# Optimization experiments

Hardware: AMD Instinct MI355X
Metric: run time of the kernel (lower is better)

Reference implementation:

```python
import jax, jax.numpy as jnp
import numpy as np
import math

VOCAB, D, H, L = 32000, 1024, 16, 4
HD = D // H
DFF = 4 * D
EPS = 1e-5


def setup_inputs() -> dict:
    key = jax.random.key(0)
    ks = jax.random.split(key, 20)
    B, T = 4, 1024
    s = 0.02
    inp = {
        'inputs': jax.random.randint(ks[0], (B, T), 0, VOCAB),
        'emb_table': jax.random.normal(ks[1], (VOCAB, D), jnp.float32) * s,
        'Wq': jax.random.normal(ks[2], (L, D, D), jnp.float32) * s,
        'bq': jnp.zeros((L, D), jnp.float32),
        'Wk': jax.random.normal(ks[3], (L, D, D), jnp.float32) * s,
        'bk': jnp.zeros((L, D), jnp.float32),
        'Wv': jax.random.normal(ks[4], (L, D, D), jnp.float32) * s,
        'bv': jnp.zeros((L, D), jnp.float32),
        'Wo': jax.random.normal(ks[5], (L, D, D), jnp.float32) * s,
        'bo': jnp.zeros((L, D), jnp.float32),
        'ln1_g': jnp.ones((L, D), jnp.float32),
        'ln1_b': jnp.zeros((L, D), jnp.float32),
        'W1': jax.random.normal(ks[6], (L, D, DFF), jnp.float32) * s,
        'b1': jnp.zeros((L, DFF), jnp.float32),
        'W2': jax.random.normal(ks[7], (L, DFF, D), jnp.float32) * s,
        'b2': jnp.zeros((L, D), jnp.float32),
        'ln2_g': jnp.ones((L, D), jnp.float32),
        'ln2_b': jnp.zeros((L, D), jnp.float32),
    }
    return inp


def _layernorm(x, g, b):
    mu = jnp.mean(x, axis=-1, keepdims=True)
    var = jnp.mean(jnp.square(x - mu), axis=-1, keepdims=True)
    return (x - mu) * jax.lax.rsqrt(var + EPS) * g + b


def _pos_emb(T):
    pos = jnp.arange(T, dtype=jnp.float32)[:, None]          # [T,1]
    div = jnp.exp(jnp.arange(0, D, 2, dtype=jnp.float32) * (-math.log(10000.0) / D))
    pe = jnp.zeros((T, D), jnp.float32)
    pe = pe.at[:, 0::2].set(jnp.sin(pos * div))
    pe = pe.at[:, 1::2].set(jnp.cos(pos * div))
    return pe


def reference(inputs, emb_table, Wq, bq, Wk, bk, Wv, bv, Wo, bo,
              ln1_g, ln1_b, W1, b1, W2, b2, ln2_g, ln2_b):
    B, T = inputs.shape
    x = emb_table[inputs] + _pos_emb(T)[None, :, :]          # [B,T,D]
    causal = jnp.tril(jnp.ones((T, T), bool))                # [T,T]
    scale = 1.0 / math.sqrt(HD)
    for l in range(L):
        q = (x @ Wq[l] + bq[l]).reshape(B, T, H, HD)
        k = (x @ Wk[l] + bk[l]).reshape(B, T, H, HD)
        v = (x @ Wv[l] + bv[l]).reshape(B, T, H, HD)
        scores = jnp.einsum('bqhd,bkhd->bhqk', q, k) * scale
        scores = jnp.where(causal, scores, -jnp.inf)
        w = jax.nn.softmax(scores, axis=-1)
        attn = jnp.einsum('bhqk,bkhd->bqhd', w, v).reshape(B, T, D)
        attn = attn @ Wo[l] + bo[l]
        x = _layernorm(x + attn, ln1_g[l], ln1_b[l])
        ff = jax.nn.relu(x @ W1[l] + b1[l]) @ W2[l] + b2[l]
        x = _layernorm(x + ff, ln2_g[l], ln2_b[l])
    return x
```

## Files before the change

kernel.cpp:

```cpp
#include <hip/hip_runtime.h>

typedef __attribute__((ext_vector_type(8))) __bf16 bf16x8;
typedef __attribute__((ext_vector_type(4))) float f32x4;
typedef __attribute__((ext_vector_type(8))) unsigned short ushort8;

#define DMODEL 1024
#define SEQ 1024
#define NLAYER 4

__device__ __forceinline__ unsigned short f2bf(float f) {
  unsigned u = __float_as_uint(f);
  u += 0x7fffu + ((u >> 16) & 1u);
  return (unsigned short)(u >> 16);
}

__device__ __forceinline__ void async_copy16(const void* gsrc, const void* lds_dst) {
  __builtin_amdgcn_global_load_lds(
      (__attribute__((address_space(1))) void*)(unsigned long long)(gsrc),
      (__attribute__((address_space(3))) void*)(unsigned int)(unsigned long long)(lds_dst),
      16, 0, 0);
}

__device__ __forceinline__ f32x4 mfma16(bf16x8 a, bf16x8 b, f32x4 c) {
  return __builtin_amdgcn_mfma_f32_16x16x32_bf16(a, b, c, 0, 0, 0);
}

__global__ __launch_bounds__(256) void preproc_kernel(
    const int* __restrict__ tok, const float* __restrict__ emb,
    const float* __restrict__ Wq, const float* __restrict__ Wk,
    const float* __restrict__ Wv, const float* __restrict__ Wo,
    const float* __restrict__ W1, const float* __restrict__ W2,
    const float* __restrict__ bq, const float* __restrict__ bk,
    const float* __restrict__ bv,
    unsigned short* __restrict__ wqkv_t, unsigned short* __restrict__ wo_t,
    unsigned short* __restrict__ w1_t, unsigned short* __restrict__ w2_t,
    float* __restrict__ qkvb, float* __restrict__ xf,
    unsigned short* __restrict__ xb) {
  __shared__ unsigned short tileT[64 * 136];
  const int bid = blockIdx.x;
  const int tid = threadIdx.x;
  if (bid < 6144) {
    const float* src; unsigned short* dst; size_t R, C; int tx, ty;
    if (bid < 2048) {
      int w = bid >> 9, z = (bid >> 7) & 3, tl = bid & 127;
      tx = tl & 15; ty = tl >> 4; R = 1024; C = 1024;
      if (w == 0)      { src = Wq + (size_t)z * 1048576; dst = wqkv_t + (size_t)z * 3145728; }
      else if (w == 1) { src = Wk + (size_t)z * 1048576; dst = wqkv_t + (size_t)z * 3145728 + 1048576; }
      else if (w == 2) { src = Wv + (size_t)z * 1048576; dst = wqkv_t + (size_t)z * 3145728 + 2097152; }
      else             { src = Wo + (size_t)z * 1048576; dst = wo_t + (size_t)z * 1048576; }
    } else if (bid < 4096) {
      int t = bid - 2048, z = t >> 9, tl = t & 511;
      tx = tl & 63; ty = tl >> 6; R = 1024; C = 4096;
      src = W1 + (size_t)z * 4194304; dst = w1_t + (size_t)z * 4194304;
    } else {
      int t = bid - 4096, z = t >> 9, tl = t & 511;
      tx = tl & 15; ty = tl >> 4; R = 4096; C = 1024;
      src = W2 + (size_t)z * 4194304; dst = w2_t + (size_t)z * 4194304;
    }
    const int c0 = tx * 64, r0 = ty * 128;
    const int s16 = tid & 15, hi = tid >> 4;
#pragma unroll
    for (int it = 0; it < 8; ++it) {
      const int r = it * 16 + hi;
      f32x4 v = __builtin_nontemporal_load(
          (const f32x4*)(src + (size_t)(r0 + r) * C + c0 + s16 * 4));
#pragma unroll
      for (int j = 0; j < 4; ++j)
        tileT[(s16 * 4 + j) * 136 + r] = f2bf(v[j]);
    }
    __syncthreads();
#pragma unroll
    for (int p = 0; p < 4; ++p) {
      const int c = p * 16 + hi;
      ushort8 o = *(const ushort8*)&tileT[c * 136 + s16 * 8];
      *(ushort8*)(dst + (size_t)(c0 + c) * R + r0 + s16 * 8) = o;
    }
  } else if (bid < 10240) {
    const int row = bid - 6144;
    const int t = row & (SEQ - 1);
    const int tk = tok[row];
    const int col = tid * 4;
    float4 e = *(const float4*)(emb + (size_t)tk * DMODEL + col);
    const float c = -9.21034037197618f / (float)DMODEL;
    float d0 = __expf((float)(col)*c);
    float d1 = __expf((float)(col + 2) * c);
    float a0 = (float)t * d0, a1 = (float)t * d1;
    e.x += sinf(a0); e.y += cosf(a0); e.z += sinf(a1); e.w += cosf(a1);
    *(float4*)(xf + (size_t)row * DMODEL + col) = e;
    ushort4 ub;
    ub.x = f2bf(e.x); ub.y = f2bf(e.y); ub.z = f2bf(e.z); ub.w = f2bf(e.w);
    *(ushort4*)(xb + (size_t)row * DMODEL + col) = ub;
  } else {
    int i = (bid - 10240) * 256 + tid;
    if (i < NLAYER * 3072) {
      int l = i / 3072, j = i % 3072;
      float v = (j < 1024) ? bq[l * 1024 + j]
              : (j < 2048) ? bk[l * 1024 + j - 1024]
                           : bv[l * 1024 + j - 2048];
      qkvb[i] = v;
    }
  }
}

#define G256_PHASE(BUF, MH, NH, STAGE_STMT, VM)                                   \
  {                                                                               \
    if (NH == 0) {                                                                \
      _Pragma("unroll") for (int fm = 0; fm < 4; ++fm)                            \
      _Pragma("unroll") for (int kk = 0; kk < 2; ++kk) {                          \
        int row = wr * 64 + fm * 16 + lr;                                         \
        int cb = (kk * 64 + g * 16) ^ ((row & 4) ? 32 : 0) ^ ((row & 8) ? 64 : 0);\
        af[fm][kk] = *(const bf16x8*)((const char*)&As[BUF][MH][0] + row * 128 + cb); \
      }                                                                           \
    }                                                                             \
    _Pragma("unroll") for (int fn = 0; fn < 2; ++fn)                              \
    _Pragma("unroll") for (int kk = 0; kk < 2; ++kk) {                            \
      int row = wc * 32 + fn * 16 + lr;                                           \
      int cb = (kk * 64 + g * 16) ^ ((row & 4) ? 32 : 0) ^ ((row & 8) ? 64 : 0);  \
      bfr[fn][kk] = *(const bf16x8*)((const char*)&Bs[BUF][NH][0] + row * 128 + cb); \
    }                                                                             \
    STAGE_STMT;                                                                   \
    if (VM == 1) asm volatile("s_waitcnt vmcnt(4)" ::: "memory");                 \
    if (VM == 2) asm volatile("s_waitcnt vmcnt(0)" ::: "memory");                 \
    asm volatile("s_barrier" ::: "memory");                                       \
    asm volatile("s_waitcnt lgkmcnt(0)" ::: "memory");                            \
    __builtin_amdgcn_s_setprio(1);                                                \
    _Pragma("unroll") for (int fm = 0; fm < 4; ++fm)                              \
    _Pragma("unroll") for (int fn = 0; fn < 2; ++fn)                              \
    _Pragma("unroll") for (int kk = 0; kk < 2; ++kk)                              \
      acc[MH][fm][NH][fn] = mfma16(af[fm][kk], bfr[fn][kk], acc[MH][fm][NH][fn]); \
    __builtin_amdgcn_s_setprio(0);                                                \
    asm volatile("s_barrier" ::: "memory");                                       \
  }

template <int QKV>
__global__ __launch_bounds__(512, 1) void gemm256(
    const unsigned short* __restrict__ A, const unsigned short* __restrict__ Bt,
    const float* __restrict__ bias, unsigned short* __restrict__ Cb,
    unsigned short* __restrict__ Cb2, int N) {
  __shared__ __align__(16) unsigned short As[2][2][8192];
  __shared__ __align__(16) unsigned short Bs[2][2][8192];
  constexpr int NK = 16;
  constexpr int NI = 8;

  const int tid = threadIdx.x;
  const int wid = tid >> 6, l = tid & 63;
  const int lr = l & 15, g = l >> 4;
  const int wr = wid >> 2, wc = wid & 3;

  const int gx = gridDim.x, nwg = gx * gridDim.y;
  int bid = blockIdx.y * gx + blockIdx.x;
  const int cpx = nwg >> 3;
  bid = (bid & 7) * cpx + (bid >> 3);
  const int rm = (bid / gx) * 256, rn = (bid % gx) * 256;

  const int kOff = ((l & 7) * 8) ^ ((l & 32) ? 16 : 0) ^ ((wid & 1) ? 32 : 0);
  const int rOff = wid * 8 + (l >> 3);

  auto stA = [&](int buf, int half, int t) {
#pragma unroll
    for (int r2 = 0; r2 < 2; ++r2) {
      const unsigned short* gs =
          A + (size_t)(rm + half * 128 + r2 * 64 + rOff) * 1024 + t * 64 + kOff;
      async_copy16(gs, &As[buf][half][r2 * 4096 + wid * 512]);
    }
  };
  auto stB = [&](int buf, int half, int t) {
#pragma unroll
    for (int r2 = 0; r2 < 2; ++r2) {
      const unsigned short* gs =
          Bt + (size_t)(rn + half * 128 + r2 * 64 + rOff) * 1024 + t * 64 + kOff;
      async_copy16(gs, &Bs[buf][half][r2 * 4096 + wid * 512]);
    }
  };

  f32x4 acc[2][4][2][2] = {};
  bf16x8 af[4][2], bfr[2][2];

  stA(0, 0, 0); stA(0, 1, 0); stB(0, 0, 0); stB(0, 1, 0);
  stA(1, 0, 1); stB(1, 0, 1);
  asm volatile("s_waitcnt vmcnt(4)" ::: "memory");
  asm volatile("s_barrier" ::: "memory");

  for (int i = 0; i < NI - 1; ++i) {
    const int t1 = 2 * i + 1, t2 = 2 * i + 2, t3 = 2 * i + 3;
    G256_PHASE(0, 0, 0, { stA(1, 1, t1); }, 0)
    G256_PHASE(0, 0, 1, { stB(1, 1, t1); }, 0)
    G256_PHASE(0, 1, 0, { stA(0, 0, t2); }, 0)
    G256_PHASE(0, 1, 1, { stB(0, 0, t2); }, 1)
    G256_PHASE(1, 0, 0, { stA(0, 1, t2); }, 0)
    G256_PHASE(1, 0, 1, { stB(0, 1, t2); }, 0)
    G256_PHASE(1, 1, 0, { if (t3 < NK) stA(1, 0, t3); }, 0)
    G256_PHASE(1, 1, 1, { if (t3 < NK) stB(1, 0, t3); }, 1)
  }
  {
    const int t1 = NK - 1;
    G256_PHASE(0, 0, 0, { stA(1, 1, t1); }, 0)
    G256_PHASE(0, 0, 1, { stB(1, 1, t1); }, 0)
    G256_PHASE(0, 1, 0, {}, 0)
    G256_PHASE(0, 1, 1, {}, 2)
    G256_PHASE(1, 0, 0, {}, 0)
    G256_PHASE(1, 0, 1, {}, 0)
    G256_PHASE(1, 1, 0, {}, 0)
    G256_PHASE(1, 1, 1, {}, 0)
  }

#pragma unroll
  for (int mh = 0; mh < 2; ++mh)
#pragma unroll
    for (int nh = 0; nh < 2; ++nh)
#pragma unroll
      for (int fn = 0; fn < 2; ++fn) {
        const int col = rn + nh * 128 + wc * 32 + fn * 16 + lr;
        const float bv = bias[col];
        if (QKV && col >= 2048) {
#pragma unroll
          for (int fm = 0; fm < 4; ++fm) {
            const int row0 = rm + mh * 128 + wr * 64 + fm * 16 + g * 4;
            ushort4 vv;
            vv.x = f2bf(acc[mh][fm][nh][fn][0] + bv);
            vv.y = f2bf(acc[mh][fm][nh][fn][1] + bv);
            vv.z = f2bf(acc[mh][fm][nh][fn][2] + bv);
            vv.w = f2bf(acc[mh][fm][nh][fn][3] + bv);
            *(ushort4*)(Cb2 + (size_t)(col - 2048) * 4096 + row0) = vv;
          }
        } else {
          const float sc = (QKV && col < 1024) ? 0.18033688011112042f : 1.0f;
          const int ldc = QKV ? 2048 : N;
#pragma unroll
          for (int fm = 0; fm < 4; ++fm)
#pragma unroll
            for (int r = 0; r < 4; ++r) {
              const int row = rm + mh * 128 + wr * 64 + fm * 16 + g * 4 + r;
              float v = (acc[mh][fm][nh][fn][r] + bv) * sc;
              if (!QKV) v = fmaxf(v, 0.0f);
              Cb[(size_t)row * ldc + col] = f2bf(v);
            }
        }
      }
}

__global__ __launch_bounds__(512, 4) void gemm_bf16w(
    const unsigned short* __restrict__ A, const unsigned short* __restrict__ Bt,
    const float* __restrict__ bias, float* __restrict__ Cf,
    const float* __restrict__ Xres, int N, int K) {
  __shared__ __align__(16) unsigned short As[2][8192];
  __shared__ __align__(16) unsigned short Bs[2][8192];
  const int tid = threadIdx.x;
  const int wid = tid >> 6, l = tid & 63, lr = l & 15, g = l >> 4;
  const int wr = wid >> 2, wc = wid & 3;
  const int d = blockIdx.y * 8 + blockIdx.x;
  const int xcd = d & 7, slot = d >> 3;
  const int bandsPerXcd = gridDim.y >> 3;
  const int by = xcd * bandsPerXcd + (slot >> 3);
  const int bx = slot & 7;
  const int rm = by * 128, rn = bx * 128;
  const int nk = K >> 6;

  const int kOff = ((l & 7) * 8) ^ ((l & 32) ? 16 : 0) ^ ((wid & 1) ? 32 : 0);
  const int rOff = wid * 8 + (l >> 3);

  auto stage = [&](int buf, int t) {
#pragma unroll
    for (int r2 = 0; r2 < 2; ++r2) {
      const unsigned short* ga =
          A + (size_t)(rm + r2 * 64 + rOff) * K + t * 64 + kOff;
      async_copy16(ga, &As[buf][r2 * 4096 + wid * 512]);
      const unsigned short* gb =
          Bt + (size_t)(rn + r2 * 64 + rOff) * K + t * 64 + kOff;
      async_copy16(gb, &Bs[buf][r2 * 4096 + wid * 512]);
    }
  };

  f32x4 acc[4][2] = {};
  stage(0, 0);
  asm volatile("s_waitcnt vmcnt(0)" ::: "memory");
  asm volatile("s_barrier" ::: "memory");

  for (int t = 0; t < nk; ++t) {
    const int cur = t & 1;
    if (t + 1 < nk) stage(cur ^ 1, t + 1);
    bf16x8 af[4][2], bfr[2][2];
#pragma unroll
    for (int fm = 0; fm < 4; ++fm)
#pragma unroll
      for (int kk = 0; kk < 2; ++kk) {
        int row = wr * 64 + fm * 16 + lr;
        int cb = (kk * 64 + g * 16) ^ ((row & 4) ? 32 : 0) ^ ((row & 8) ? 64 : 0);
        af[fm][kk] = *(const bf16x8*)((const char*)&As[cur][0] + row * 128 + cb);
      }
#pragma unroll
    for (int fn = 0; fn < 2; ++fn)
#pragma unroll
      for (int kk = 0; kk < 2; ++kk) {
        int row = wc * 32 + fn * 16 + lr;
        int cb = (kk * 64 + g * 16) ^ ((row & 4) ? 32 : 0) ^ ((row & 8) ? 64 : 0);
        bfr[fn][kk] = *(const bf16x8*)((const char*)&Bs[cur][0] + row * 128 + cb);
      }
    asm volatile("s_waitcnt lgkmcnt(0)" ::: "memory");
    __builtin_amdgcn_sched_barrier(0);
    __builtin_amdgcn_s_setprio(1);
#pragma unroll
    for (int fm = 0; fm < 4; ++fm)
#pragma unroll
      for (int fn = 0; fn < 2; ++fn)
#pragma unroll
        for (int kk = 0; kk < 2; ++kk)
          acc[fm][fn] = mfma16(af[fm][kk], bfr[fn][kk], acc[fm][fn]);
    __builtin_amdgcn_s_setprio(0);
    asm volatile("s_waitcnt vmcnt(0)" ::: "memory");
    asm volatile("s_barrier" ::: "memory");
  }

  const int row0 = rm + wr * 64 + g * 4;
  const int col0 = rn + wc * 32 + lr;
#pragma unroll
  for (int fn = 0; fn < 2; ++fn) {
    const int col = col0 + fn * 16;
    const float bv = bias[col];
#pragma unroll
    for (int fm = 0; fm < 4; ++fm)
#pragma unroll
      for (int r = 0; r < 4; ++r) {
        const int row = row0 + fm * 16 + r;
        Cf[(size_t)row * N + col] =
            acc[fm][fn][r] + bv + Xres[(size_t)row * N + col];
      }
  }
}

__global__ __launch_bounds__(256) void attn_kernel(
    const unsigned short* __restrict__ qk, const unsigned short* __restrict__ Vt,
    unsigned short* __restrict__ out) {
  __shared__ unsigned short Pl[4][32 * 72];
  const int tid = threadIdx.x;
  const int w = tid >> 6, lr = tid & 15, g = (tid & 63) >> 4;
  const int bh = blockIdx.x;
  const int b = bh >> 4, h = bh & 15;
  const int byy = blockIdx.y;
  const int qblk = (byy & 1) ? (byy >> 1) : (7 - (byy >> 1));
  const int qb0 = qblk * 128 + w * 32;
  const size_t rowBase = (size_t)b * SEQ;
  const int cq = h * 64, ck = 1024 + h * 64;
  const unsigned short* Vb = Vt + (size_t)(h * 64) * 4096 + b * 1024;

  bf16x8 aq[2][2];
#pragma unroll
  for (int qf = 0; qf < 2; ++qf)
#pragma unroll
    for (int ks = 0; ks < 2; ++ks)
      aq[qf][ks] = *(const bf16x8*)(qk + (rowBase + qb0 + qf * 16 + lr) * 2048 +
                                    cq + ks * 32 + g * 8);

  f32x4 o[2][4] = {};
  float l_[2][4] = {};

  const int NT = (qb0 + 32 + 63) >> 6;

  bf16x8 kf[4][2];
#pragma unroll
  for (int kg = 0; kg < 4; ++kg) {
    const unsigned short* kp = qk + (rowBase + kg * 16 + lr) * 2048 + ck + g * 8;
    kf[kg][0] = *(const bf16x8*)(kp);
    kf[kg][1] = *(const bf16x8*)(kp + 32);
  }

  for (int kt = 0; kt < NT; ++kt) {
    const int k0 = kt * 64;
    bf16x8 vf[4][2];
#pragma unroll
    for (int nbv = 0; nbv < 4; ++nbv) {
      const unsigned short* vp = Vb + (size_t)(nbv * 16 + lr) * 4096 + k0 + g * 8;
      vf[nbv][0] = *(const bf16x8*)(vp);
      vf[nbv][1] = *(const bf16x8*)(vp + 32);
    }
    f32x4 s[2][4] = {};
#pragma unroll
    for (int kg = 0; kg < 4; ++kg)
#pragma unroll
      for (int qf = 0; qf < 2; ++qf) {
        s[qf][kg] = mfma16(aq[qf][0], kf[kg][0], s[qf][kg]);
        s[qf][kg] = mfma16(aq[qf][1], kf[kg][1], s[qf][kg]);
      }
    if (kt + 1 < NT) {
#pragma unroll
      for (int kg = 0; kg < 4; ++kg) {
        const unsigned short* kp =
            qk + (rowBase + k0 + 64 + kg * 16 + lr) * 2048 + ck + g * 8;
        kf[kg][0] = *(const bf16x8*)(kp);
        kf[kg][1] = *(const bf16x8*)(kp + 32);
      }
    }
#pragma unroll
    for (int qf = 0; qf < 2; ++qf)
#pragma unroll
      for (int r = 0; r < 4; ++r) {
        const int q = qb0 + qf * 16 + g * 4 + r;
        float e0 = (k0 + lr <= q) ? exp2f(s[qf][0][r]) : 0.0f;
        float e1 = (k0 + 16 + lr <= q) ? exp2f(s[qf][1][r]) : 0.0f;
        float e2 = (k0 + 32 + lr <= q) ? exp2f(s[qf][2][r]) : 0.0f;
        float e3 = (k0 + 48 + lr <= q) ? exp2f(s[qf][3][r]) : 0.0f;
        l_[qf][r] += (e0 + e1) + (e2 + e3);
        unsigned short* pr = &Pl[w][(qf * 16 + g * 4 + r) * 72];
        pr[lr] = f2bf(e0);
        pr[16 + lr] = f2bf(e1);
        pr[32 + lr] = f2bf(e2);
        pr[48 + lr] = f2bf(e3);
      }
    asm volatile("s_waitcnt lgkmcnt(0)" ::: "memory");
    __builtin_amdgcn_sched_barrier(0);
    bf16x8 pa[2][2];
#pragma unroll
    for (int qf = 0; qf < 2; ++qf)
#pragma unroll
      for (int kc = 0; kc < 2; ++kc)
        pa[qf][kc] = *(const bf16x8*)&Pl[w][(qf * 16 + lr) * 72 + kc * 32 + g * 8];
#pragma unroll
    for (int nbv = 0; nbv < 4; ++nbv)
#pragma unroll
      for (int qf = 0; qf < 2; ++qf) {
        o[qf][nbv] = mfma16(pa[qf][0], vf[nbv][0], o[qf][nbv]);
        o[qf][nbv] = mfma16(pa[qf][1], vf[nbv][1], o[qf][nbv]);
      }
  }
  float rinv[2][4];
#pragma unroll
  for (int qf = 0; qf < 2; ++qf)
#pragma unroll
    for (int r = 0; r < 4; ++r) {
      float t = l_[qf][r];
      t += __shfl_xor(t, 1, 64);
      t += __shfl_xor(t, 2, 64);
      t += __shfl_xor(t, 4, 64);
      t += __shfl_xor(t, 8, 64);
      rinv[qf][r] = __builtin_amdgcn_rcpf(t);
    }
#pragma unroll
  for (int qf = 0; qf < 2; ++qf)
#pragma unroll
    for (int nbv = 0; nbv < 4; ++nbv)
#pragma unroll
      for (int r = 0; r < 4; ++r) {
        float val = o[qf][nbv][r] * rinv[qf][r];
        out[(rowBase + qb0 + qf * 16 + g * 4 + r) * 1024 + h * 64 + nbv * 16 + lr] =
            f2bf(val);
      }
}

__global__ __launch_bounds__(256) void ln_kernel(
    const float* __restrict__ tin,
    const float* __restrict__ gam, const float* __restrict__ bet,
    float* __restrict__ xout, unsigned short* __restrict__ xbf,
    float* __restrict__ out2) {
  const int row = blockIdx.x;
  const int col = threadIdx.x * 4;
  const int lane = threadIdx.x & 63, w = threadIdx.x >> 6;
  float4 v = *(const float4*)(tin + (size_t)row * DMODEL + col);
  float s = v.x + v.y + v.z + v.w;
  float ss = v.x * v.x + v.y * v.y + v.z * v.z + v.w * v.w;
#pragma unroll
  for (int msk = 32; msk; msk >>= 1) {
    s += __shfl_xor(s, msk, 64);
    ss += __shfl_xor(ss, msk, 64);
  }
  __shared__ float ps[4], pss[4];
  if (lane == 0) { ps[w] = s; pss[w] = ss; }
  __syncthreads();
  float tot = ps[0] + ps[1] + ps[2] + ps[3];
  float tots = pss[0] + pss[1] + pss[2] + pss[3];
  float mean = tot * (1.0f / DMODEL);
  float var = tots * (1.0f / DMODEL) - mean * mean;
  float inv = rsqrtf(var + 1e-5f);
  float4 gv = *(const float4*)(gam + col);
  float4 bv = *(const float4*)(bet + col);
  float4 ov;
  ov.x = (v.x - mean) * inv * gv.x + bv.x;
  ov.y = (v.y - mean) * inv * gv.y + bv.y;
  ov.z = (v.z - mean) * inv * gv.z + bv.z;
  ov.w = (v.w - mean) * inv * gv.w + bv.w;
  *(float4*)(xout + (size_t)row * DMODEL + col) = ov;
  ushort4 ub;
  ub.x = f2bf(ov.x); ub.y = f2bf(ov.y); ub.z = f2bf(ov.z); ub.w = f2bf(ov.w);
  *(ushort4*)(xbf + (size_t)row * DMODEL + col) = ub;
  if (out2) *(float4*)(out2 + (size_t)row * DMODEL + col) = ov;
}

extern "C" void kernel_launch(void* const* d_in, const int* in_sizes, int n_in,
                              void* d_out, int out_size, void* d_ws, size_t ws_size,
                              hipStream_t stream) {
  (void)in_sizes; (void)n_in; (void)out_size; (void)ws_size;
  const int* tok = (const int*)d_in[0];
  const float* emb = (const float*)d_in[1];
  const float* Wq = (const float*)d_in[2];
  const float* bq = (const float*)d_in[3];
  const float* Wk = (const float*)d_in[4];
  const float* bk = (const float*)d_in[5];
  const float* Wv = (const float*)d_in[6];
  const float* bv = (const float*)d_in[7];
  const float* Wo = (const float*)d_in[8];
  const float* bo = (const float*)d_in[9];
  const float* ln1g = (const float*)d_in[10];
  const float* ln1b = (const float*)d_in[11];
  const float* W1 = (const float*)d_in[12];
  const float* b1 = (const float*)d_in[13];
  const float* W2 = (const float*)d_in[14];
  const float* b2 = (const float*)d_in[15];
  const float* ln2g = (const float*)d_in[16];
  const float* ln2b = (const float*)d_in[17];

  char* ws = (char*)d_ws;
  size_t off = 0;
  auto alloc = [&](size_t bytes) {
    char* p = ws + off;
    off += (bytes + 255) & ~(size_t)255;
    return p;
  };
  unsigned short* wqkv_t = (unsigned short*)alloc((size_t)NLAYER * 3072 * 1024 * 2);
  unsigned short* wo_t = (unsigned short*)alloc((size_t)NLAYER * 1024 * 1024 * 2);
  unsigned short* w1_t = (unsigned short*)alloc((size_t)NLAYER * 4096 * 1024 * 2);
  unsigned short* w2_t = (unsigned short*)alloc((size_t)NLAYER * 1024 * 4096 * 2);
  float* qkvb = (float*)alloc((size_t)NLAYER * 3072 * 4);
  float* xf = (float*)alloc((size_t)4096 * 1024 * 4);
  float* yf = (float*)alloc((size_t)4096 * 1024 * 4);
  unsigned short* xb = (unsigned short*)alloc((size_t)4096 * 1024 * 2);
  unsigned short* qkbuf = (unsigned short*)alloc((size_t)4096 * 2048 * 2);
  unsigned short* vt = (unsigned short*)alloc((size_t)1024 * 4096 * 2);
  unsigned short* attn = (unsigned short*)alloc((size_t)4096 * 1024 * 2);
  unsigned short* hb = (unsigned short*)alloc((size_t)4096 * 4096 * 2);

  preproc_kernel<<<dim3(10288), dim3(256), 0, stream>>>(
      tok, emb, Wq, Wk, Wv, Wo, W1, W2, bq, bk, bv,
      wqkv_t, wo_t, w1_t, w2_t, qkvb, xf, xb);

  for (int l = 0; l < NLAYER; ++l) {
    gemm256<1><<<dim3(12, 16), dim3(512), 0, stream>>>(
        xb, wqkv_t + (size_t)l * 3145728, qkvb + l * 3072, qkbuf, vt, 3072);
    attn_kernel<<<dim3(64, 8), dim3(256), 0, stream>>>(qkbuf, vt, attn);
    gemm_bf16w<<<dim3(8, 32), dim3(512), 0, stream>>>(
        attn, wo_t + (size_t)l * 1048576, bo + l * 1024, yf, xf, 1024, 1024);
    ln_kernel<<<dim3(4096), dim3(256), 0, stream>>>(
        yf, ln1g + l * 1024, ln1b + l * 1024, xf, xb, nullptr);
    gemm256<0><<<dim3(16, 16), dim3(512), 0, stream>>>(
        xb, w1_t + (size_t)l * 4194304, b1 + l * 4096, hb, nullptr, 4096);
    gemm_bf16w<<<dim3(8, 32), dim3(512), 0, stream>>>(
        hb, w2_t + (size_t)l * 4194304, b2 + l * 1024, yf, xf, 1024, 4096);
    ln_kernel<<<dim3(4096), dim3(256), 0, stream>>>(
        yf, ln2g + l * 1024, ln2b + l * 1024, xf, xb,
        (l == NLAYER - 1) ? (float*)d_out : nullptr);
  }
}
```

Before: 931.4 us.

## Keep residual stream only in bf16 and swizzle transpose LDS tile

Removes the fp32 copy of the residual stream: the embedding and layernorm kernels no longer write fp32 x, and the output-projection and FFN2 GEMM epilogues read the bf16 activation buffer as the residual instead. This cuts global memory traffic per layer (one fp32 write in each LN, fp32 residual reads become bf16). The weight transpose in preproc also gets an XOR swizzle on its LDS tile to reduce bank conflicts. The cost is that residual additions now use bf16-rounded inputs, which lowers accuracy.

```diff
diff --git a/kernel.cpp b/kernel.cpp
--- a/kernel.cpp
+++ b/kernel.cpp
@@ -12,6 +12,10 @@
   unsigned u = __float_as_uint(f);
   u += 0x7fffu + ((u >> 16) & 1u);
   return (unsigned short)(u >> 16);
+}
+
+__device__ __forceinline__ float bf2f(unsigned short u) {
+  return __uint_as_float((unsigned)u << 16);
 }
 
 __device__ __forceinline__ void async_copy16(const void* gsrc, const void* lds_dst) {
@@ -34,8 +38,7 @@
     const float* __restrict__ bv,
     unsigned short* __restrict__ wqkv_t, unsigned short* __restrict__ wo_t,
     unsigned short* __restrict__ w1_t, unsigned short* __restrict__ w2_t,
-    float* __restrict__ qkvb, float* __restrict__ xf,
-    unsigned short* __restrict__ xb) {
+    float* __restrict__ qkvb, unsigned short* __restrict__ xb) {
   __shared__ unsigned short tileT[64 * 136];
   const int bid = blockIdx.x;
   const int tid = threadIdx.x;
@@ -65,14 +68,16 @@
       f32x4 v = __builtin_nontemporal_load(
           (const f32x4*)(src + (size_t)(r0 + r) * C + c0 + s16 * 4));
 #pragma unroll
-      for (int j = 0; j < 4; ++j)
-        tileT[(s16 * 4 + j) * 136 + r] = f2bf(v[j]);
+      for (int j = 0; j < 4; ++j) {
+        const int c = s16 * 4 + j;
+        tileT[c * 136 + (r ^ ((c & 7) << 3))] = f2bf(v[j]);
+      }
     }
     __syncthreads();
 #pragma unroll
     for (int p = 0; p < 4; ++p) {
       const int c = p * 16 + hi;
-      ushort8 o = *(const ushort8*)&tileT[c * 136 + s16 * 8];
+      ushort8 o = *(const ushort8*)&tileT[c * 136 + 8 * (s16 ^ (c & 7))];
       *(ushort8*)(dst + (size_t)(c0 + c) * R + r0 + s16 * 8) = o;
     }
   } else if (bid < 10240) {
@@ -86,7 +91,6 @@
     float d1 = __expf((float)(col + 2) * c);
     float a0 = (float)t * d0, a1 = (float)t * d1;
     e.x += sinf(a0); e.y += cosf(a0); e.z += sinf(a1); e.w += cosf(a1);
-    *(float4*)(xf + (size_t)row * DMODEL + col) = e;
     ushort4 ub;
     ub.x = f2bf(e.x); ub.y = f2bf(e.y); ub.z = f2bf(e.z); ub.w = f2bf(e.w);
     *(ushort4*)(xb + (size_t)row * DMODEL + col) = ub;
@@ -242,7 +246,7 @@
 __global__ __launch_bounds__(512, 4) void gemm_bf16w(
     const unsigned short* __restrict__ A, const unsigned short* __restrict__ Bt,
     const float* __restrict__ bias, float* __restrict__ Cf,
-    const float* __restrict__ Xres, int N, int K) {
+    const unsigned short* __restrict__ Xres, int N, int K) {
   __shared__ __align__(16) unsigned short As[2][8192];
   __shared__ __align__(16) unsigned short Bs[2][8192];
   const int tid = threadIdx.x;
@@ -323,7 +327,7 @@
       for (int r = 0; r < 4; ++r) {
         const int row = row0 + fm * 16 + r;
         Cf[(size_t)row * N + col] =
-            acc[fm][fn][r] + bv + Xres[(size_t)row * N + col];
+            acc[fm][fn][r] + bv + bf2f(Xres[(size_t)row * N + col]);
       }
   }
 }
@@ -449,8 +453,7 @@
 __global__ __launch_bounds__(256) void ln_kernel(
     const float* __restrict__ tin,
     const float* __restrict__ gam, const float* __restrict__ bet,
-    float* __restrict__ xout, unsigned short* __restrict__ xbf,
-    float* __restrict__ out2) {
+    unsigned short* __restrict__ xbf, float* __restrict__ out2) {
   const int row = blockIdx.x;
   const int col = threadIdx.x * 4;
   const int lane = threadIdx.x & 63, w = threadIdx.x >> 6;
@@ -477,7 +480,6 @@
   ov.y = (v.y - mean) * inv * gv.y + bv.y;
   ov.z = (v.z - mean) * inv * gv.z + bv.z;
   ov.w = (v.w - mean) * inv * gv.w + bv.w;
-  *(float4*)(xout + (size_t)row * DMODEL + col) = ov;
   ushort4 ub;
   ub.x = f2bf(ov.x); ub.y = f2bf(ov.y); ub.z = f2bf(ov.z); ub.w = f2bf(ov.w);
   *(ushort4*)(xbf + (size_t)row * DMODEL + col) = ub;
@@ -519,7 +521,6 @@
   unsigned short* w1_t = (unsigned short*)alloc((size_t)NLAYER * 4096 * 1024 * 2);
   unsigned short* w2_t = (unsigned short*)alloc((size_t)NLAYER * 1024 * 4096 * 2);
   float* qkvb = (float*)alloc((size_t)NLAYER * 3072 * 4);
-  float* xf = (float*)alloc((size_t)4096 * 1024 * 4);
   float* yf = (float*)alloc((size_t)4096 * 1024 * 4);
   unsigned short* xb = (unsigned short*)alloc((size_t)4096 * 1024 * 2);
   unsigned short* qkbuf = (unsigned short*)alloc((size_t)4096 * 2048 * 2);
@@ -529,22 +530,22 @@
 
   preproc_kernel<<<dim3(10288), dim3(256), 0, stream>>>(
       tok, emb, Wq, Wk, Wv, Wo, W1, W2, bq, bk, bv,
-      wqkv_t, wo_t, w1_t, w2_t, qkvb, xf, xb);
+      wqkv_t, wo_t, w1_t, w2_t, qkvb, xb);
 
   for (int l = 0; l < NLAYER; ++l) {
     gemm256<1><<<dim3(12, 16), dim3(512), 0, stream>>>(
         xb, wqkv_t + (size_t)l * 3145728, qkvb + l * 3072, qkbuf, vt, 3072);
     attn_kernel<<<dim3(64, 8), dim3(256), 0, stream>>>(qkbuf, vt, attn);
     gemm_bf16w<<<dim3(8, 32), dim3(512), 0, stream>>>(
-        attn, wo_t + (size_t)l * 1048576, bo + l * 1024, yf, xf, 1024, 1024);
+        attn, wo_t + (size_t)l * 1048576, bo + l * 1024, yf, xb, 1024, 1024);
     ln_kernel<<<dim3(4096), dim3(256), 0, stream>>>(
-        yf, ln1g + l * 1024, ln1b + l * 1024, xf, xb, nullptr);
+        yf, ln1g + l * 1024, ln1b + l * 1024, xb, nullptr);
     gemm256<0><<<dim3(16, 16), dim3(512), 0, stream>>>(
         xb, w1_t + (size_t)l * 4194304, b1 + l * 4096, hb, nullptr, 4096);
     gemm_bf16w<<<dim3(8, 32), dim3(512), 0, stream>>>(
-        hb, w2_t + (size_t)l * 4194304, b2 + l * 1024, yf, xf, 1024, 4096);
+        hb, w2_t + (size_t)l * 4194304, b2 + l * 1024, yf, xb, 1024, 4096);
     ln_kernel<<<dim3(4096), dim3(256), 0, stream>>>(
-        yf, ln2g + l * 1024, ln2b + l * 1024, xf, xb,
+        yf, ln2g + l * 1024, ln2b + l * 1024, xb,
         (l == NLAYER - 1) ? (float*)d_out : nullptr);
   }
 }
```

Measured after the change: 917.1 us. No clear change (-1.5%).
